# Optimization experiments

Measured on AMD Instinct MI355X. Metric: run time of the kernel, lower is better.

Reference implementation:

```python
import jax, jax.numpy as jnp
import numpy as np
from jax import lax

T, B, F, H, C = 1024, 128, 88, 1024, 88


def setup_inputs() -> dict:
    key = jax.random.key(0)
    ks = jax.random.split(key, 8)
    s = 0.02
    lengths = jnp.sort(jax.random.randint(ks[1], (B,), 1, T + 1))[::-1]  # descending, as pack_padded requires
    return {
        "input_sequences": jax.random.normal(ks[0], (T, B, F), dtype=jnp.float32),
        "input_sequence_lengths": lengths.astype(jnp.int64),
        "W_ih": jax.random.normal(ks[2], (4 * H, F), dtype=jnp.float32) * s,
        "W_hh": jax.random.normal(ks[3], (4 * H, H), dtype=jnp.float32) * s,
        "b_ih": jax.random.normal(ks[4], (4 * H,), dtype=jnp.float32) * s,
        "b_hh": jax.random.normal(ks[5], (4 * H,), dtype=jnp.float32) * s,
        "W_fc": jax.random.normal(ks[6], (C, H), dtype=jnp.float32) * s,
        "b_fc": jax.random.normal(ks[7], (C,), dtype=jnp.float32) * s,
    }


def reference(input_sequences, input_sequence_lengths, W_ih, W_hh, b_ih, b_hh, W_fc, b_fc):
    Tn, Bn, _ = input_sequences.shape
    Hn = W_hh.shape[1]
    # mask[t, b] = True iff timestep t is within sequence b (equivalent to :batch_size_t slicing
    # when lengths are sorted descending, as the torch code assumes)
    mask_seq = jnp.arange(Tn)[:, None] < input_sequence_lengths[None, :]  # [T, B]

    h0 = jnp.zeros((Bn, Hn), dtype=input_sequences.dtype)
    c0 = jnp.zeros((Bn, Hn), dtype=input_sequences.dtype)

    def step(carry, inp):
        h, c = carry
        x, m = inp  # x: [B, F], m: [B]
        gates = x @ W_ih.T + b_ih + h @ W_hh.T + b_hh  # [B, 4H], order i,f,g,o
        i, f, g, o = jnp.split(gates, 4, axis=1)
        c_new = jax.nn.sigmoid(f) * c + jax.nn.sigmoid(i) * jnp.tanh(g)
        h_new = jax.nn.sigmoid(o) * jnp.tanh(c_new)
        mb = m[:, None]
        h2 = jnp.where(mb, h_new, h)
        c2 = jnp.where(mb, c_new, c)
        logits_t = jnp.where(mb, h2 @ W_fc.T + b_fc, 0.0)  # rows beyond batch_size_t stay zero
        return (h2, c2), logits_t

    (_, _), predictions = lax.scan(step, (h0, c0), (input_sequences, mask_seq))  # [T, B, C]

    logits = jnp.transpose(predictions, (1, 0, 2))  # [B, T, C]
    binary_logits = jnp.stack((logits, 1.0 - logits), axis=3)  # [B, T, C, 2]
    return binary_logits.reshape(-1, 2)
```

## Files before the change

### kernel.cpp

```cpp
#include <hip/hip_runtime.h>
#include <cstdint>
#include <cstddef>

#define T_STEPS 1024
#define B_SZ    128
#define F_SZ    88
#define H_SZ    1024
#define C_SZ    88

#define N_GATE_WG 128
#define N_FC_WG   3
#define N_COMPUTE (N_GATE_WG + N_FC_WG)
#define N_WG      (N_COMPUTE + 1)
#define BLOCK     256
#define FLAG_STRIDE 16
#define RING      16

typedef __attribute__((ext_vector_type(8)))  __bf16 bf16x8;
typedef __attribute__((ext_vector_type(16))) float  f32x16;
typedef __attribute__((ext_vector_type(4)))  int    i32x4;

#define SLAB_OFF    0
#define SLAB_BYTES  (70 * 512 * 2)
#define BIAS_OFF    (SLAB_OFF + SLAB_BYTES)
#define LENL_OFF    (BIAS_OFF + 128)
#define NB_OFF      (LENL_OFF + 512)
#define EXCH_OFF    (NB_OFF + 2064)
#define EXCH_WAVE   (16 * 68 * 4)
#define EXCH_BYTES  (4 * EXCH_WAVE)
#define STAGE_OFF   (EXCH_OFF + EXCH_BYTES)
#define STAGE_BYTES (4 * 32 * 8 * 2)
#define SMEM_BYTES  (STAGE_OFF + STAGE_BYTES)

#define HBUF_ELEMS  131072
#define HBUF_BYTES  (HBUF_ELEMS * 2)

#define BCAST_IDX   (136 * FLAG_STRIDE)

__device__ __forceinline__ float sigm(float x) {
    return __builtin_amdgcn_rcpf(1.0f + __expf(-x));
}
__device__ __forceinline__ float tanh_fast(float x) {
    return 1.0f - 2.0f * __builtin_amdgcn_rcpf(__expf(2.0f * x) + 1.0f);
}
__device__ __forceinline__ void st_llc(void* p, uint64_t v) {
    __hip_atomic_store((uint64_t*)p, v, __ATOMIC_RELAXED,
                       __HIP_MEMORY_SCOPE_AGENT);
}

extern "C" __global__ void __launch_bounds__(BLOCK, 1)
lstm_fused(const float* __restrict__ X,
           const int*   __restrict__ len_raw,
           const float* __restrict__ W_ih,
           const float* __restrict__ W_hh,
           const float* __restrict__ b_ih,
           const float* __restrict__ b_hh,
           const float* __restrict__ W_fc,
           const float* __restrict__ b_fc,
           float*       __restrict__ out,
           __bf16*      __restrict__ hbuf,
           int*         __restrict__ flags)
{
    extern __shared__ char smem[];
    __bf16*         slab  = (__bf16*)(smem + SLAB_OFF);
    float*          biasL = (float*)(smem + BIAS_OFF);
    int*            lenL  = (int*)(smem + LENL_OFF);
    unsigned short* nbL   = (unsigned short*)(smem + NB_OFF);

    const int  wg   = blockIdx.x;
    const int  tid  = threadIdx.x;
    const int  w    = tid >> 6;
    const int  lane = tid & 63;
    const int  col  = lane & 31;
    const int  h5   = lane >> 5;
    const bool isGate   = (wg < N_GATE_WG);
    const bool isMaster = (wg == N_COMPUTE);

    const int lstride = (len_raw[1] == 0) ? 2 : 1;
    if (tid < B_SZ) lenL[tid] = len_raw[tid * lstride];
    __syncthreads();
    for (int t = tid; t <= T_STEPS; t += BLOCK) {
        int cnt = 0;
        #pragma unroll 4
        for (int b = 0; b < B_SZ; ++b) cnt += (lenL[b] > t) ? 1 : 0;
        nbL[t] = (unsigned short)cnt;
    }

    if (isGate) {
        const int j0 = wg * 8;
        for (int idx = tid; idx < 32 * 1024; idx += BLOCK) {
            int cc = idx >> 10, k = idx & 1023;
            int gate = cc & 3, u = cc >> 2;
            float v = W_hh[(size_t)(gate * H_SZ + j0 + u) * H_SZ + k];
            slab[((k >> 4) * 64 + ((k >> 3) & 1) * 32 + cc) * 8 + (k & 7)] = (__bf16)v;
        }
        for (int idx = tid; idx < 32 * 96; idx += BLOCK) {
            int cc = idx & 31, k = idx >> 5;
            int gate = cc & 3, u = cc >> 2;
            float v = (k < F_SZ) ? W_ih[(size_t)(gate * H_SZ + j0 + u) * F_SZ + k] : 0.0f;
            slab[((64 + (k >> 4)) * 64 + ((k >> 3) & 1) * 32 + cc) * 8 + (k & 7)] = (__bf16)v;
        }
        if (tid < 32) {
            int gate = tid & 3, u = tid >> 2;
            int row = gate * H_SZ + j0 + u;
            biasL[tid] = b_ih[row] + b_hh[row];
        }
    } else if (!isMaster) {
        const int c0 = (wg - N_GATE_WG) * 32;
        for (int idx = tid; idx < 32 * 1024; idx += BLOCK) {
            int cc = idx >> 10, k = idx & 1023;
            int c = c0 + cc;
            float v = (c < C_SZ) ? W_fc[(size_t)c * H_SZ + k] : 0.0f;
            slab[((k >> 4) * 64 + ((k >> 3) & 1) * 32 + cc) * 8 + (k & 7)] = (__bf16)v;
        }
        if (tid < 32) {
            int c = c0 + tid;
            biasL[tid] = (c < C_SZ) ? b_fc[c] : 0.0f;
        }
    }

    __syncthreads();
    if (tid == 0 && !isMaster) {
        __builtin_amdgcn_s_waitcnt(0);
        __hip_atomic_store(flags + wg * FLAG_STRIDE, 1, __ATOMIC_RELAXED,
                           __HIP_MEMORY_SCOPE_AGENT);
    }

    if (isMaster) {
        if (w != 0) return;
        const bool has2 = (128 + lane) < N_COMPUTE;
        long g = 0;
        for (int t = 0; t <= T_STEPS; ++t) {
            const int target = t + 1;
            for (;;) {
                int a = __hip_atomic_load(flags + lane * FLAG_STRIDE,
                                          __ATOMIC_RELAXED, __HIP_MEMORY_SCOPE_AGENT);
                int b = __hip_atomic_load(flags + (64 + lane) * FLAG_STRIDE,
                                          __ATOMIC_RELAXED, __HIP_MEMORY_SCOPE_AGENT);
                int c = has2 ? __hip_atomic_load(flags + (128 + lane) * FLAG_STRIDE,
                                                 __ATOMIC_RELAXED, __HIP_MEMORY_SCOPE_AGENT)
                             : target;
                if (__all((a >= target) && (b >= target) && (c >= target))) break;
                __builtin_amdgcn_s_sleep(1);
                if (++g > 400000000L) break;
            }
            if (lane == 0)
                __hip_atomic_store(flags + BCAST_IDX, target, __ATOMIC_RELAXED,
                                   __HIP_MEMORY_SCOPE_AGENT);
        }
        return;
    }

    float c_reg[4] = {0.f, 0.f, 0.f, 0.f};
    float h_reg[4] = {0.f, 0.f, 0.f, 0.f};

    const int g4    = col & 3;
    const int ktile = wg >> 1;
    const int half  = wg & 1;
    const int u0    = col >> 2;
    const int c0fc  = (wg - N_GATE_WG) * 32;
    const int phase = wg & (RING - 1);

    float*  exch   = (float*)(smem + EXCH_OFF) + w * (EXCH_WAVE / 4);
    __bf16* stageW = (__bf16*)(smem + STAGE_OFF) + w * 256;

    long guard = 0;

    for (int t = 0; t <= T_STEPS; ++t) {
        const int nb_t   = (t < T_STEPS) ? (int)nbL[t] : 0;
        const int nb_pre = (t > 0) ? (int)nbL[t - 1] : B_SZ;
        const __bf16* hin  = hbuf + (size_t)((t + RING - 1) & (RING - 1)) * HBUF_ELEMS;
        __bf16*       hout = hbuf + (size_t)(t & (RING - 1)) * HBUF_ELEMS;

        const bool gcomp = isGate && (t < T_STEPS) && (w * 32 < nb_t);
        const bool gwrt  = isGate && (t < T_STEPS) && (w * 32 < nb_pre);

        f32x16 acc;

        if (gcomp) {
            float bv = biasL[col];
            #pragma unroll
            for (int i = 0; i < 16; ++i) acc[i] = bv;
            const float* xrow = X + ((size_t)t * B_SZ + (w * 32 + col)) * F_SZ;
            #pragma unroll
            for (int kt = 0; kt < 6; ++kt) {
                int f0 = kt * 16 + h5 * 8;
                bf16x8 a;
                if (f0 < F_SZ) {
                    float4 lo = *(const float4*)(xrow + f0);
                    float4 hi = *(const float4*)(xrow + f0 + 4);
                    a[0] = (__bf16)lo.x; a[1] = (__bf16)lo.y; a[2] = (__bf16)lo.z; a[3] = (__bf16)lo.w;
                    a[4] = (__bf16)hi.x; a[5] = (__bf16)hi.y; a[6] = (__bf16)hi.z; a[7] = (__bf16)hi.w;
                } else {
                    #pragma unroll
                    for (int j = 0; j < 8; ++j) a[j] = (__bf16)0.0f;
                }
                bf16x8 b = __builtin_bit_cast(bf16x8,
                    *(const i32x4*)(slab + (size_t)(64 + kt) * 512 + lane * 8));
                acc = __builtin_amdgcn_mfma_f32_32x32x16_bf16(a, b, acc, 0, 0, 0);
            }
        }

        {
            const int target = t + 1;
            for (;;) {
                int v = __hip_atomic_load(flags + BCAST_IDX, __ATOMIC_RELAXED,
                                          __HIP_MEMORY_SCOPE_AGENT);
                if (v >= target) break;
                __builtin_amdgcn_s_sleep(1);
                if (++guard > 400000000L) break;
            }
        }
        __syncthreads();

        if (((t + phase) & (RING - 1)) == 0) {
            if (tid == 0)
                __builtin_amdgcn_fence(__ATOMIC_ACQUIRE, "agent");
            __syncthreads();
        }

        if (!isGate && tid == 0) {
            __hip_atomic_store(flags + wg * FLAG_STRIDE, t + 2, __ATOMIC_RELAXED,
                               __HIP_MEMORY_SCOPE_AGENT);
        }

        if (!isGate && t >= 1) {
            const int  s        = t - 1;
            const int  nb_s     = (int)nbL[s];
            const bool act_tile = (w * 32) < nb_s;
            #pragma unroll
            for (int i = 0; i < 16; ++i) acc[i] = 0.0f;
            if (act_tile) {
                float bv = biasL[col];
                #pragma unroll
                for (int i = 0; i < 16; ++i) acc[i] = bv;
                const __bf16* hA = hin + (size_t)(w * 64 + lane) * 8;
                const __bf16* bB = slab + lane * 8;
                #pragma unroll 8
                for (int kt = 0; kt < 64; ++kt) {
                    bf16x8 a = __builtin_bit_cast(bf16x8, *(const i32x4*)(hA + (size_t)kt * 2048));
                    bf16x8 b = __builtin_bit_cast(bf16x8, *(const i32x4*)(bB + (size_t)kt * 512));
                    acc = __builtin_amdgcn_mfma_f32_32x32x16_bf16(a, b, acc, 0, 0, 0);
                }
            }
            const int c = c0fc + col;
            if (c < C_SZ) {
                #pragma unroll
                for (int i = 0; i < 16; ++i) {
                    int row = (i & 3) + 8 * (i >> 2) + 4 * h5;
                    int b   = w * 32 + row;
                    float v = (act_tile && b < nb_s) ? acc[i] : 0.0f;
                    float2 o2; o2.x = v; o2.y = 1.0f - v;
                    *(float2*)(out + ((size_t)(b * T_STEPS + s) * C_SZ + c) * 2) = o2;
                }
            }
        }

        if (gcomp && t > 0) {
            const __bf16* hA = hin + (size_t)(w * 64 + lane) * 8;
            const __bf16* bB = slab + lane * 8;
            i32x4 pf0[16], pf1[16];
            #pragma unroll
            for (int i = 0; i < 16; ++i)
                pf0[i] = *(const i32x4*)(hA + (size_t)i * 2048);
            __builtin_amdgcn_sched_barrier(0);
            #pragma unroll
            for (int c = 0; c < 4; ++c) {
                i32x4 (&cur)[16] = (c & 1) ? pf1 : pf0;
                i32x4 (&nxt)[16] = (c & 1) ? pf0 : pf1;
                if (c < 3) {
                    #pragma unroll
                    for (int i = 0; i < 16; ++i)
                        nxt[i] = *(const i32x4*)(hA + (size_t)((c + 1) * 16 + i) * 2048);
                }
                __builtin_amdgcn_sched_barrier(0);
                #pragma unroll
                for (int i = 0; i < 16; ++i) {
                    bf16x8 a = __builtin_bit_cast(bf16x8, cur[i]);
                    bf16x8 b = __builtin_bit_cast(bf16x8,
                        *(const i32x4*)(bB + (size_t)(c * 16 + i) * 512));
                    acc = __builtin_amdgcn_mfma_f32_32x32x16_bf16(a, b, acc, 0, 0, 0);
                }
                __builtin_amdgcn_sched_barrier(0);
            }
        }
        if (gcomp) {
            #pragma unroll
            for (int j = 0; j < 16; ++j) exch[j * 68 + lane] = acc[j];
        }
        __syncthreads();

        if (gcomp) {
            #pragma unroll
            for (int q = 0; q < 4; ++q) {
                const float4 v = *(const float4*)(exch + (4 * g4 + q) * 68 + 32 * h5 + (col & ~3));
                float si = sigm(v.x);
                float sf = sigm(v.y);
                float tg = tanh_fast(v.z);
                float so = sigm(v.w);
                float cn = sf * c_reg[q] + si * tg;
                float hn = so * tanh_fast(cn);
                int row = 8 * g4 + 4 * h5 + q;
                int b   = w * 32 + row;
                if (b < nb_t) { c_reg[q] = cn; h_reg[q] = hn; }
            }
        }
        if (gwrt) {
            #pragma unroll
            for (int q = 0; q < 4; ++q) {
                int row = 8 * g4 + 4 * h5 + q;
                stageW[row * 8 + u0] = (__bf16)h_reg[q];
            }
        }
        __syncthreads();

        if (gwrt && h5 == half) {
            const uint64_t* sp = (const uint64_t*)(stageW + col * 8);
            uint64_t* hp = (uint64_t*)(hout + (size_t)((ktile * 4 + w) * 64 + half * 32 + col) * 8);
            st_llc(hp,     sp[0]);
            st_llc(hp + 1, sp[1]);
        }
        __syncthreads();

        if (isGate && tid == 0) {
            __builtin_amdgcn_s_waitcnt(0);
            __hip_atomic_store(flags + wg * FLAG_STRIDE, t + 2, __ATOMIC_RELAXED,
                               __HIP_MEMORY_SCOPE_AGENT);
        }
    }
}

extern "C" void kernel_launch(void* const* d_in, const int* in_sizes, int n_in,
                              void* d_out, int out_size, void* d_ws, size_t ws_size,
                              hipStream_t stream) {
    const float* X    = (const float*)d_in[0];
    const int*   lens = (const int*)d_in[1];
    const float* Wih  = (const float*)d_in[2];
    const float* Whh  = (const float*)d_in[3];
    const float* bih  = (const float*)d_in[4];
    const float* bhh  = (const float*)d_in[5];
    const float* Wfc  = (const float*)d_in[6];
    const float* bfc  = (const float*)d_in[7];
    float*       outp = (float*)d_out;

    __bf16* hbuf  = (__bf16*)d_ws;
    int*    flags = (int*)((char*)d_ws + (size_t)RING * HBUF_BYTES);

    (void)hipFuncSetAttribute((const void*)lstm_fused,
                              hipFuncAttributeMaxDynamicSharedMemorySize, SMEM_BYTES);

    void* args[] = { (void*)&X, (void*)&lens, (void*)&Wih, (void*)&Whh,
                     (void*)&bih, (void*)&bhh, (void*)&Wfc, (void*)&bfc,
                     (void*)&outp, (void*)&hbuf, (void*)&flags };
    (void)hipLaunchCooperativeKernel((void*)lstm_fused, dim3(N_WG), dim3(BLOCK),
                                     args, (unsigned)SMEM_BYTES, stream);
}
```

Before: 8.197 ms.

## Replace master-workgroup barrier with decentralized per-workgroup flag polling

Removes the dedicated master workgroup that gathered all completion flags and broadcast a single step counter. Each compute workgroup's wave 0 now polls all 131 per-workgroup flags directly before every timestep. This drops one hop of cross-workgroup latency from every step of the global barrier. In exchange, every workgroup now generates polling traffic on all flags, which adds memory contention. It also adds a fallback to a normal launch if the cooperative launch fails.

After: 8.570 ms. 1.05x slower.

```diff
diff --git a/kernel.cpp b/kernel.cpp
--- a/kernel.cpp
+++ b/kernel.cpp
@@ -11,7 +11,7 @@
 #define N_GATE_WG 128
 #define N_FC_WG   3
 #define N_COMPUTE (N_GATE_WG + N_FC_WG)
-#define N_WG      (N_COMPUTE + 1)
+#define N_WG      N_COMPUTE
 #define BLOCK     256
 #define FLAG_STRIDE 16
 #define RING      16
@@ -34,8 +34,6 @@
 
 #define HBUF_ELEMS  131072
 #define HBUF_BYTES  (HBUF_ELEMS * 2)
-
-#define BCAST_IDX   (136 * FLAG_STRIDE)
 
 __device__ __forceinline__ float sigm(float x) {
     return __builtin_amdgcn_rcpf(1.0f + __expf(-x));
@@ -73,8 +71,7 @@
     const int  lane = tid & 63;
     const int  col  = lane & 31;
     const int  h5   = lane >> 5;
-    const bool isGate   = (wg < N_GATE_WG);
-    const bool isMaster = (wg == N_COMPUTE);
+    const bool isGate = (wg < N_GATE_WG);
 
     const int lstride = (len_raw[1] == 0) ? 2 : 1;
     if (tid < B_SZ) lenL[tid] = len_raw[tid * lstride];
@@ -105,7 +102,7 @@
             int row = gate * H_SZ + j0 + u;
             biasL[tid] = b_ih[row] + b_hh[row];
         }
-    } else if (!isMaster) {
+    } else {
         const int c0 = (wg - N_GATE_WG) * 32;
         for (int idx = tid; idx < 32 * 1024; idx += BLOCK) {
             int cc = idx >> 10, k = idx & 1023;
@@ -120,17 +117,64 @@
     }
 
     __syncthreads();
-    if (tid == 0 && !isMaster) {
+    if (tid == 0) {
         __builtin_amdgcn_s_waitcnt(0);
         __hip_atomic_store(flags + wg * FLAG_STRIDE, 1, __ATOMIC_RELAXED,
                            __HIP_MEMORY_SCOPE_AGENT);
     }
 
-    if (isMaster) {
-        if (w != 0) return;
-        const bool has2 = (128 + lane) < N_COMPUTE;
-        long g = 0;
-        for (int t = 0; t <= T_STEPS; ++t) {
+    float c_reg[4] = {0.f, 0.f, 0.f, 0.f};
+    float h_reg[4] = {0.f, 0.f, 0.f, 0.f};
+
+    const int g4    = col & 3;
+    const int ktile = wg >> 1;
+    const int half  = wg & 1;
+    const int u0    = col >> 2;
+    const int c0fc  = (wg - N_GATE_WG) * 32;
+    const int phase = wg & (RING - 1);
+
+    float*  exch   = (float*)(smem + EXCH_OFF) + w * (EXCH_WAVE / 4);
+    __bf16* stageW = (__bf16*)(smem + STAGE_OFF) + w * 256;
+
+    const bool has2 = (128 + lane) < N_COMPUTE;
+    long guard = 0;
+
+    for (int t = 0; t <= T_STEPS; ++t) {
+        const int nb_t   = (t < T_STEPS) ? (int)nbL[t] : 0;
+        const int nb_pre = (t > 0) ? (int)nbL[t - 1] : B_SZ;
+        const __bf16* hin  = hbuf + (size_t)((t + RING - 1) & (RING - 1)) * HBUF_ELEMS;
+        __bf16*       hout = hbuf + (size_t)(t & (RING - 1)) * HBUF_ELEMS;
+
+        const bool gcomp = isGate && (t < T_STEPS) && (w * 32 < nb_t);
+        const bool gwrt  = isGate && (t < T_STEPS) && (w * 32 < nb_pre);
+
+        f32x16 acc;
+
+        if (gcomp) {
+            float bv = biasL[col];
+            #pragma unroll
+            for (int i = 0; i < 16; ++i) acc[i] = bv;
+            const float* xrow = X + ((size_t)t * B_SZ + (w * 32 + col)) * F_SZ;
+            #pragma unroll
+            for (int kt = 0; kt < 6; ++kt) {
+                int f0 = kt * 16 + h5 * 8;
+                bf16x8 a;
+                if (f0 < F_SZ) {
+                    float4 lo = *(const float4*)(xrow + f0);
+                    float4 hi = *(const float4*)(xrow + f0 + 4);
+                    a[0] = (__bf16)lo.x; a[1] = (__bf16)lo.y; a[2] = (__bf16)lo.z; a[3] = (__bf16)lo.w;
+                    a[4] = (__bf16)hi.x; a[5] = (__bf16)hi.y; a[6] = (__bf16)hi.z; a[7] = (__bf16)hi.w;
+                } else {
+                    #pragma unroll
+                    for (int j = 0; j < 8; ++j) a[j] = (__bf16)0.0f;
+                }
+                bf16x8 b = __builtin_bit_cast(bf16x8,
+                    *(const i32x4*)(slab + (size_t)(64 + kt) * 512 + lane * 8));
+                acc = __builtin_amdgcn_mfma_f32_32x32x16_bf16(a, b, acc, 0, 0, 0);
+            }
+        }
+
+        if (w == 0) {
             const int target = t + 1;
             for (;;) {
                 int a = __hip_atomic_load(flags + lane * FLAG_STRIDE,
@@ -142,72 +186,6 @@
                              : target;
                 if (__all((a >= target) && (b >= target) && (c >= target))) break;
                 __builtin_amdgcn_s_sleep(1);
-                if (++g > 400000000L) break;
-            }
-            if (lane == 0)
-                __hip_atomic_store(flags + BCAST_IDX, target, __ATOMIC_RELAXED,
-                                   __HIP_MEMORY_SCOPE_AGENT);
-        }
-        return;
-    }
-
-    float c_reg[4] = {0.f, 0.f, 0.f, 0.f};
-    float h_reg[4] = {0.f, 0.f, 0.f, 0.f};
-
-    const int g4    = col & 3;
-    const int ktile = wg >> 1;
-    const int half  = wg & 1;
-    const int u0    = col >> 2;
-    const int c0fc  = (wg - N_GATE_WG) * 32;
-    const int phase = wg & (RING - 1);
-
-    float*  exch   = (float*)(smem + EXCH_OFF) + w * (EXCH_WAVE / 4);
-    __bf16* stageW = (__bf16*)(smem + STAGE_OFF) + w * 256;
-
-    long guard = 0;
-
-    for (int t = 0; t <= T_STEPS; ++t) {
-        const int nb_t   = (t < T_STEPS) ? (int)nbL[t] : 0;
-        const int nb_pre = (t > 0) ? (int)nbL[t - 1] : B_SZ;
-        const __bf16* hin  = hbuf + (size_t)((t + RING - 1) & (RING - 1)) * HBUF_ELEMS;
-        __bf16*       hout = hbuf + (size_t)(t & (RING - 1)) * HBUF_ELEMS;
-
-        const bool gcomp = isGate && (t < T_STEPS) && (w * 32 < nb_t);
-        const bool gwrt  = isGate && (t < T_STEPS) && (w * 32 < nb_pre);
-
-        f32x16 acc;
-
-        if (gcomp) {
-            float bv = biasL[col];
-            #pragma unroll
-            for (int i = 0; i < 16; ++i) acc[i] = bv;
-            const float* xrow = X + ((size_t)t * B_SZ + (w * 32 + col)) * F_SZ;
-            #pragma unroll
-            for (int kt = 0; kt < 6; ++kt) {
-                int f0 = kt * 16 + h5 * 8;
-                bf16x8 a;
-                if (f0 < F_SZ) {
-                    float4 lo = *(const float4*)(xrow + f0);
-                    float4 hi = *(const float4*)(xrow + f0 + 4);
-                    a[0] = (__bf16)lo.x; a[1] = (__bf16)lo.y; a[2] = (__bf16)lo.z; a[3] = (__bf16)lo.w;
-                    a[4] = (__bf16)hi.x; a[5] = (__bf16)hi.y; a[6] = (__bf16)hi.z; a[7] = (__bf16)hi.w;
-                } else {
-                    #pragma unroll
-                    for (int j = 0; j < 8; ++j) a[j] = (__bf16)0.0f;
-                }
-                bf16x8 b = __builtin_bit_cast(bf16x8,
-                    *(const i32x4*)(slab + (size_t)(64 + kt) * 512 + lane * 8));
-                acc = __builtin_amdgcn_mfma_f32_32x32x16_bf16(a, b, acc, 0, 0, 0);
-            }
-        }
-
-        {
-            const int target = t + 1;
-            for (;;) {
-                int v = __hip_atomic_load(flags + BCAST_IDX, __ATOMIC_RELAXED,
-                                          __HIP_MEMORY_SCOPE_AGENT);
-                if (v >= target) break;
-                __builtin_amdgcn_s_sleep(1);
                 if (++guard > 400000000L) break;
             }
         }
@@ -234,7 +212,8 @@
                 float bv = biasL[col];
                 #pragma unroll
                 for (int i = 0; i < 16; ++i) acc[i] = bv;
-                const __bf16* hA = hin + (size_t)(w * 64 + lane) * 8;
+                const __bf16* hA = hbuf + (size_t)((t + RING - 1) & (RING - 1)) * HBUF_ELEMS
+                                        + (size_t)(w * 64 + lane) * 8;
                 const __bf16* bB = slab + lane * 8;
                 #pragma unroll 8
                 for (int kt = 0; kt < 64; ++kt) {
@@ -352,6 +331,11 @@
     void* args[] = { (void*)&X, (void*)&lens, (void*)&Wih, (void*)&Whh,
                      (void*)&bih, (void*)&bhh, (void*)&Wfc, (void*)&bfc,
                      (void*)&outp, (void*)&hbuf, (void*)&flags };
-    (void)hipLaunchCooperativeKernel((void*)lstm_fused, dim3(N_WG), dim3(BLOCK),
-                                     args, (unsigned)SMEM_BYTES, stream);
-}
+    hipError_t le = hipLaunchCooperativeKernel((void*)lstm_fused, dim3(N_WG), dim3(BLOCK),
+                                               args, (unsigned)SMEM_BYTES, stream);
+    if (le != hipSuccess) {
+        hipLaunchKernelGGL(lstm_fused, dim3(N_WG), dim3(BLOCK),
+                           (unsigned)SMEM_BYTES, stream,
+                           X, lens, Wih, Whh, bih, bhh, Wfc, bfc, outp, hbuf, flags);
+    }
+}
```
